# Optimization experiments

Hardware: AMD Instinct MI355X
Metric: run time of the kernel (lower is better)

## Reference

```python
import jax, jax.numpy as jnp
import numpy as np

EMB_DIM = 1024
NUM_HEADS = 16
SCALE_WEIGHTS = 1.0
TINY = jnp.finfo(jnp.float32).tiny


def setup_inputs() -> dict:
    key = jax.random.key(0)
    k1, k2, k3 = jax.random.split(key, 3)
    B, S = 2, 2048
    x = jax.random.normal(k1, (B, S, EMB_DIM), dtype=jnp.float32)
    weights = jax.random.uniform(k2, (B, S), dtype=jnp.float32)
    W_qkv = jax.random.normal(k3, (EMB_DIM, 3 * EMB_DIM), dtype=jnp.float32) / np.sqrt(EMB_DIM)
    b_qkv = jnp.zeros((3 * EMB_DIM,), dtype=jnp.float32)
    return {"x": x, "weights": weights, "W_qkv": W_qkv, "b_qkv": b_qkv}


def reference(x, weights, W_qkv, b_qkv):
    B, S, E = x.shape
    H = NUM_HEADS
    hd = E // H
    # QKV projection: [B,S,3E] -> [B,H,S,3*hd] -> split
    qkv = x @ W_qkv + b_qkv
    qkv = qkv.reshape(B, S, H, 3 * hd).transpose(0, 2, 1, 3)
    q, k, v = jnp.split(qkv, 3, axis=-1)  # each [B,H,S,hd]
    # weights: [B,S] -> [B,1,1,S] (broadcast over heads and query positions)
    w = weights[:, None, None, :]
    # scores with log-weight bias and hard masks
    attn_logits = jnp.einsum("bhqd,bhkd->bhqk", q, k) / jnp.sqrt(jnp.asarray(hd, x.dtype))
    attn_logits = attn_logits + jnp.log(w / SCALE_WEIGHTS + TINY)
    attn_logits = jnp.where(w == 0, -9e15, attn_logits)
    attn_logits = jnp.where(w == 1, 9e15, attn_logits)
    attention = jax.nn.softmax(attn_logits, axis=-1)
    values = jnp.einsum("bhqk,bhkd->bhqd", attention, v)
    return values.transpose(0, 2, 1, 3).reshape(B, S, E)
```

## Files before the change

### kernel.cpp

```cpp
#include <hip/hip_runtime.h>
#include <math.h>

#define B_  2
#define S_  2048
#define E_  1024
#define H_  16
#define HD_ 64
#define N3_ 3072
#define M_  (B_*S_)

typedef _Float16 h8  __attribute__((ext_vector_type(8)));
typedef _Float16 h4  __attribute__((ext_vector_type(4)));
typedef _Float16 h2  __attribute__((ext_vector_type(2)));
typedef __fp16   fp16x2 __attribute__((ext_vector_type(2)));
typedef float    f4  __attribute__((ext_vector_type(4)));
typedef float    fv16 __attribute__((ext_vector_type(16)));

typedef __attribute__((address_space(3))) unsigned int       lds_u32;
typedef const __attribute__((address_space(1))) unsigned int glob_u32;

__device__ __forceinline__ void gld16(const void* g, void* l) {
    __builtin_amdgcn_global_load_lds((glob_u32*)g, (lds_u32*)l, 16, 0, 0);
}
__device__ __forceinline__ float exp2_hw(float x) { return __builtin_amdgcn_exp2f(x); }
__device__ __forceinline__ float fmax3(float a, float b, float c) {
    return fmaxf(fmaxf(a, b), c);
}
__device__ __forceinline__ h2 cvt_pk_f16(float a, float b) {
    fp16x2 r = __builtin_amdgcn_cvt_pkrtz(a, b);
    return __builtin_bit_cast(h2, r);
}

#define QSCALE 0.18033688011112042f
#define RESCALE_THR 8.0f

__global__ __launch_bounds__(256) void prep_kernel(
        const float* __restrict__ x, _Float16* __restrict__ x16,
        const float* __restrict__ w, _Float16* __restrict__ w16,
        const float* __restrict__ W, _Float16* __restrict__ Wt) {
    __shared__ float T[64][65];
    int L = blockIdx.x;
    int tid = threadIdx.x;
    if (L < 2050) {
        const float* src = (L < 2048) ? &x[(size_t)L * 2048] : &w[(size_t)(L - 2048) * 2048];
        _Float16* dst    = (L < 2048) ? &x16[(size_t)L * 2048] : &w16[(size_t)(L - 2048) * 2048];
        int i = tid * 8;
        float4 u = *(const float4*)&src[i];
        float4 v = *(const float4*)&src[i + 4];
        h8 o;
        o[0] = (_Float16)u.x; o[1] = (_Float16)u.y; o[2] = (_Float16)u.z; o[3] = (_Float16)u.w;
        o[4] = (_Float16)v.x; o[5] = (_Float16)v.y; o[6] = (_Float16)v.z; o[7] = (_Float16)v.w;
        *(h8*)&dst[i] = o;
    } else {
        int L2 = L - 2050;
        int k0 = (L2 & 15) * 64, n0 = (L2 >> 4) * 64;
        int r = tid >> 4, c4 = (tid & 15) * 4;
#pragma unroll
        for (int i = 0; i < 4; i++) {
            int row = r + i * 16;
            float4 u = *(const float4*)&W[(size_t)(k0 + row) * N3_ + n0 + c4];
            T[c4 + 0][row] = u.x; T[c4 + 1][row] = u.y;
            T[c4 + 2][row] = u.z; T[c4 + 3][row] = u.w;
        }
        __syncthreads();
#pragma unroll
        for (int i = 0; i < 4; i++) {
            int rn = r + i * 16;
            h4 p;
            p[0] = (_Float16)T[rn][c4 + 0]; p[1] = (_Float16)T[rn][c4 + 1];
            p[2] = (_Float16)T[rn][c4 + 2]; p[3] = (_Float16)T[rn][c4 + 3];
            *(h4*)&Wt[(size_t)(n0 + rn) * E_ + k0 + c4] = p;
        }
    }
}

__global__ __launch_bounds__(256, 2) void qkv_gemm32(
        const _Float16* __restrict__ x16, const _Float16* __restrict__ wt,
        const float* __restrict__ bq, const float* __restrict__ w,
        _Float16* __restrict__ qws, _Float16* __restrict__ kws,
        _Float16* __restrict__ vtws) {
    __shared__ __align__(16) _Float16 Ab[2][128 * 64];
    __shared__ __align__(16) _Float16 Wb[2][192 * 64];

    int tid = threadIdx.x;
    int wid = tid >> 6, lane = tid & 63;
    int l31 = lane & 31, hi = lane >> 5, l7 = l31 & 7;
    int srow = lane >> 3;
    int wm = wid & 1, wn = wid >> 1;

    int L = blockIdx.x;
    int xcd = L & 7;
    int idx = L >> 3;
    int head = (xcd & 1) * 8 + (idx & 7);
    int mb   = (xcd >> 1) * 8 + (idx >> 3);
    int m0 = mb * 128;
    int n0 = head * 192;
    int b = m0 >> 11;
    int bh = b * H_ + head;
    int sblk = m0 & 2047;

    fv16 acc[2][3];
#pragma unroll
    for (int ntl = 0; ntl < 3; ntl++) {
        int n_abs = wn * 96 + ntl * 32;
        int which = n_abs >> 6;
        fv16 ini;
        if (which == 2) {
            float bb = bq[n0 + n_abs + l31];
#pragma unroll
            for (int r = 0; r < 16; r++) ini[r] = bb;
        } else {
#pragma unroll
            for (int g = 0; g < 4; g++) {
                f4 bv = *(const f4*)&bq[n0 + n_abs + 8 * g + 4 * hi];
#pragma unroll
                for (int j = 0; j < 4; j++) ini[4 * g + j] = bv[j];
            }
        }
        acc[0][ntl] = ini; acc[1][ntl] = ini;
    }

    auto stage = [&](int t, int bf) {
        int k0 = t * 64;
#pragma unroll
        for (int j = 0; j < 4; j++) {
            int batch = wid * 4 + j;
            int row = batch * 8 + srow;
            int ch = (lane & 7) ^ srow ^ (batch & 7);
            gld16(&x16[(size_t)(m0 + row) * E_ + k0 + ch * 8], &Ab[bf][batch * 8 * 64]);
        }
#pragma unroll
        for (int j = 0; j < 6; j++) {
            int batch = wid * 6 + j;
            int row = batch * 8 + srow;
            int ch = (lane & 7) ^ srow ^ (batch & 7);
            gld16(&wt[(size_t)(n0 + row) * E_ + k0 + ch * 8], &Wb[bf][batch * 8 * 64]);
        }
    };

    stage(0, 0);

    for (int t = 0; t < 16; t++) {
        int bf = t & 1;
        __syncthreads();
        if (t < 15) stage(t + 1, bf ^ 1);
#pragma unroll
        for (int step = 0; step < 4; step++) {
            h8 af[2], wf[3];
#pragma unroll
            for (int mt = 0; mt < 2; mt++) {
                int R = wm * 64 + mt * 32 + l31;
                int ph = ((2 * step + hi) ^ l7 ^ ((mt * 4 + (l31 >> 3)) & 7)) * 8;
                af[mt] = *(const h8*)&Ab[bf][R * 64 + ph];
            }
#pragma unroll
            for (int ntl = 0; ntl < 3; ntl++) {
                int R = wn * 96 + ntl * 32 + l31;
                int ph = ((2 * step + hi) ^ l7 ^ ((wn * 12 + ntl * 4 + (l31 >> 3)) & 7)) * 8;
                wf[ntl] = *(const h8*)&Wb[bf][R * 64 + ph];
            }
#pragma unroll
            for (int ntl = 0; ntl < 3; ntl++) {
                bool isv = (wn == 1) && (ntl >= 1);
#pragma unroll
                for (int mt = 0; mt < 2; mt++) {
                    if (isv)
                        acc[mt][ntl] = __builtin_amdgcn_mfma_f32_32x32x16_f16(af[mt], wf[ntl], acc[mt][ntl], 0, 0, 0);
                    else
                        acc[mt][ntl] = __builtin_amdgcn_mfma_f32_32x32x16_f16(wf[ntl], af[mt], acc[mt][ntl], 0, 0, 0);
                }
            }
        }
    }

#pragma unroll
    for (int ntl = 0; ntl < 3; ntl++) {
        int n_abs = wn * 96 + ntl * 32;
        int which = n_abs >> 6;
#pragma unroll
        for (int mt = 0; mt < 2; mt++) {
            if (which == 2) {
                int d = (n_abs & 63) + l31;
#pragma unroll
                for (int g = 0; g < 4; g++) {
                    int soff = wm * 64 + mt * 32 + 8 * g + 4 * hi;
                    f4 wf4 = *(const f4*)&w[m0 + soff];
                    h4 p;
#pragma unroll
                    for (int j = 0; j < 4; j++)
                        p[j] = (_Float16)(acc[mt][ntl][4 * g + j] * wf4[j]);
                    *(h4*)&vtws[((size_t)bh * 64 + d) * S_ + sblk + soff] = p;
                }
            } else {
                _Float16* dst = (which == 0) ? qws : kws;
                float scale = (which == 0) ? QSCALE : 1.0f;
                int s = sblk + wm * 64 + mt * 32 + l31;
#pragma unroll
                for (int g = 0; g < 4; g++) {
                    int d0 = (n_abs & 63) + 8 * g + 4 * hi;
                    h4 p;
#pragma unroll
                    for (int j = 0; j < 4; j++)
                        p[j] = (_Float16)(acc[mt][ntl][4 * g + j] * scale);
                    *(h4*)&dst[((size_t)bh * S_ + s) * 64 + d0] = p;
                }
            }
        }
    }
}

__global__ __launch_bounds__(256, 2) void attn_kernel(
        const _Float16* __restrict__ q, const _Float16* __restrict__ k,
        const _Float16* __restrict__ vt, const _Float16* __restrict__ w16,
        float* __restrict__ out) {
    __shared__ __align__(16) _Float16 Kb[2][64 * 64];
    __shared__ __align__(16) _Float16 Vb[2][64 * 64];
    __shared__ __align__(16) _Float16 lws16[2048];

    int tid = threadIdx.x;
    int wid = tid >> 6, lane = tid & 63;
    int l31 = lane & 31, hi = lane >> 5, l7 = l31 & 7;
    int srow = lane >> 3;
    int L = blockIdx.x;
    int bh = (L & 7) + 8 * (L >> 7);
    int qt = (L >> 3) & 15;
    int q0 = qt * 128;
    int b = bh >> 4, h = bh & 15;

    const _Float16* qbase = q + (size_t)bh * S_ * HD_;
    const _Float16* kbase = k + (size_t)bh * S_ * HD_;
    const _Float16* vbase = vt + (size_t)bh * HD_ * S_;
    const _Float16* wbase = w16 + (size_t)b * S_;

    gld16(&wbase[wid * 512 + lane * 8], &lws16[wid * 512]);

    auto stage = [&](int kt, int bf) {
        int k0 = kt * 64;
#pragma unroll
        for (int j = 0; j < 2; j++) {
            int batch = wid * 2 + j;
            int row = batch * 8 + srow;
            int ch = (lane & 7) ^ srow ^ (batch & 7);
            gld16(&kbase[(size_t)(k0 + row) * 64 + ch * 8], &Kb[bf][batch * 8 * 64]);
            gld16(&vbase[(size_t)row * S_ + k0 + ch * 8], &Vb[bf][batch * 8 * 64]);
        }
    };

    stage(0, 0);

    int qrow = q0 + wid * 32 + l31;
    h8 qf[4];
#pragma unroll
    for (int step = 0; step < 4; step++)
        qf[step] = *(const h8*)&qbase[(size_t)qrow * 64 + 16 * step + 8 * hi];

    fv16 o[2], ol;
    o[0] = (fv16)0.0f; o[1] = (fv16)0.0f; ol = (fv16)0.0f;
    float m_r = -INFINITY;

    for (int kt = 0; kt < 32; kt++) {
        int bf = kt & 1;
        __syncthreads();
        if (kt < 31) stage(kt + 1, bf ^ 1);

        fv16 st[2];
        st[0] = (fv16)0.0f; st[1] = (fv16)0.0f;
        __builtin_amdgcn_s_setprio(1);
#pragma unroll
        for (int step = 0; step < 4; step++) {
#pragma unroll
            for (int kt2 = 0; kt2 < 2; kt2++) {
                int R = kt2 * 32 + l31;
                int ph = ((2 * step + hi) ^ l7 ^ ((kt2 * 4 + (l31 >> 3)) & 7)) * 8;
                h8 kf = *(const h8*)&Kb[bf][R * 64 + ph];
                st[kt2] = __builtin_amdgcn_mfma_f32_32x32x16_f16(kf, qf[step], st[kt2], 0, 0, 0);
            }
        }
        __builtin_amdgcn_s_setprio(0);

        float tm[11];
#pragma unroll
        for (int r = 0; r < 10; r++)
            tm[r] = fmax3(st[(3*r)>>4][(3*r)&15], st[(3*r+1)>>4][(3*r+1)&15],
                          st[(3*r+2)>>4][(3*r+2)&15]);
        tm[10] = fmaxf(st[1][14], st[1][15]);
        float u0 = fmax3(tm[0], tm[1], tm[2]);
        float u1 = fmax3(tm[3], tm[4], tm[5]);
        float u2 = fmax3(tm[6], tm[7], tm[8]);
        float u3 = fmaxf(tm[9], tm[10]);
        float pmax = fmaxf(fmax3(u0, u1, u2), u3);

        if (!__all(pmax <= m_r + RESCALE_THR)) {
            float rowmax = fmaxf(pmax, __shfl_xor(pmax, 32));
            float mnew = fmaxf(m_r, rowmax);
            float alpha = exp2_hw(m_r - mnew);
            m_r = mnew;
            o[0] = o[0] * alpha;
            o[1] = o[1] * alpha;
            ol = ol * alpha;
        }

        h4 pf[2][4];
#pragma unroll
        for (int kt2 = 0; kt2 < 2; kt2++)
#pragma unroll
            for (int g = 0; g < 4; g++) {
                float e0 = exp2_hw(st[kt2][4 * g + 0] - m_r);
                float e1 = exp2_hw(st[kt2][4 * g + 1] - m_r);
                float e2 = exp2_hw(st[kt2][4 * g + 2] - m_r);
                float e3 = exp2_hw(st[kt2][4 * g + 3] - m_r);
                h2 p01 = cvt_pk_f16(e0, e1);
                h2 p23 = cvt_pk_f16(e2, e3);
                h4 p;
                p[0] = p01[0]; p[1] = p01[1]; p[2] = p23[0]; p[3] = p23[1];
                pf[kt2][g] = p;
            }

        int k0 = kt * 64;
        __builtin_amdgcn_s_setprio(1);
#pragma unroll
        for (int kt2 = 0; kt2 < 2; kt2++)
#pragma unroll
            for (int g = 0; g < 4; g++) {
                int c = 4 * kt2 + g;
#pragma unroll
                for (int dt = 0; dt < 2; dt++) {
                    int R = dt * 32 + l31;
                    int ph = (c ^ l7 ^ ((dt * 4 + (l31 >> 3)) & 7)) * 8 + hi * 4;
                    h4 vf = *(const h4*)&Vb[bf][R * 64 + ph];
                    o[dt] = __builtin_amdgcn_mfma_f32_32x32x8f16(vf, pf[kt2][g], o[dt], 0, 0, 0);
                }
                h4 wf_ = *(const h4*)&lws16[k0 + c * 8 + 4 * hi];
                ol = __builtin_amdgcn_mfma_f32_32x32x8f16(wf_, pf[kt2][g], ol, 0, 0, 0);
            }
        __builtin_amdgcn_s_setprio(0);
    }

    float linv = 1.0f / ol[0];
    float* obase = &out[((size_t)(b * S_ + qrow)) * E_ + h * 64];
#pragma unroll
    for (int dt = 0; dt < 2; dt++)
#pragma unroll
        for (int g = 0; g < 4; g++) {
            int d0 = dt * 32 + 8 * g + 4 * hi;
            f4 ov;
#pragma unroll
            for (int j = 0; j < 4; j++) ov[j] = o[dt][4 * g + j] * linv;
            *(f4*)&obase[d0] = ov;
        }
}

extern "C" void kernel_launch(void* const* d_in, const int* in_sizes, int n_in,
                              void* d_out, int out_size, void* d_ws, size_t ws_size,
                              hipStream_t stream) {
    const float* x  = (const float*)d_in[0];
    const float* w  = (const float*)d_in[1];
    const float* Wq = (const float*)d_in[2];
    const float* bq = (const float*)d_in[3];
    float* out = (float*)d_out;

    char* p = (char*)d_ws;
    _Float16* x16 = (_Float16*)p;              p += (size_t)M_ * E_ * 2;
    _Float16* wt  = (_Float16*)p;              p += (size_t)E_ * N3_ * 2;
    _Float16* qb  = (_Float16*)p;              p += (size_t)M_ * E_ * 2;
    _Float16* kb  = (_Float16*)p;              p += (size_t)M_ * E_ * 2;
    _Float16* vtb = (_Float16*)p;              p += (size_t)M_ * HD_ * H_ * 2;
    _Float16* w16 = (_Float16*)p;

    prep_kernel<<<dim3(2050 + 768), dim3(256), 0, stream>>>(x, x16, w, w16, Wq, wt);
    qkv_gemm32<<<dim3(512), dim3(256), 0, stream>>>(x16, wt, bq, w, qb, kb, vtb);
    attn_kernel<<<dim3(512), dim3(256), 0, stream>>>(qb, kb, vtb, w16, out);
}
```

Baseline: 177.0 us.

## Split attention KV range across two wave groups per block and merge in LDS

Doubles the attention block to 512 threads and splits the key sequence in two halves, each processed by four waves with their own double-buffered K/V LDS tiles. At the end, partial outputs, maxima and row sums from the second half are written to LDS and merged flash-decoding style by the first half. The aim is more waves in flight per CU and half the serial loop length per block, to hide latency. The cost is double the LDS footprint, an extra merge step, and a tighter register budget from the new launch bounds.

```diff
diff --git a/kernel.cpp b/kernel.cpp
--- a/kernel.cpp
+++ b/kernel.cpp
@@ -209,18 +209,20 @@
     }
 }
 
-__global__ __launch_bounds__(256, 2) void attn_kernel(
+__global__ __launch_bounds__(512, 4) void attn_kernel(
         const _Float16* __restrict__ q, const _Float16* __restrict__ k,
         const _Float16* __restrict__ vt, const _Float16* __restrict__ w16,
         float* __restrict__ out) {
-    __shared__ __align__(16) _Float16 Kb[2][64 * 64];
-    __shared__ __align__(16) _Float16 Vb[2][64 * 64];
+    __shared__ __align__(16) _Float16 Kb[2][2][64 * 64];
+    __shared__ __align__(16) _Float16 Vb[2][2][64 * 64];
     __shared__ __align__(16) _Float16 lws16[2048];
 
     int tid = threadIdx.x;
     int wid = tid >> 6, lane = tid & 63;
     int l31 = lane & 31, hi = lane >> 5, l7 = l31 & 7;
     int srow = lane >> 3;
+    int s = wid >> 2;
+    int w4 = wid & 3;
     int L = blockIdx.x;
     int bh = (L & 7) + 8 * (L >> 7);
     int qt = (L >> 3) & 15;
@@ -232,23 +234,23 @@
     const _Float16* vbase = vt + (size_t)bh * HD_ * S_;
     const _Float16* wbase = w16 + (size_t)b * S_;
 
-    gld16(&wbase[wid * 512 + lane * 8], &lws16[wid * 512]);
-
-    auto stage = [&](int kt, int bf) {
-        int k0 = kt * 64;
+    if (wid < 4) gld16(&wbase[wid * 512 + lane * 8], &lws16[wid * 512]);
+
+    auto stage = [&](int t, int bf) {
+        int k0 = (s * 16 + t) * 64;
 #pragma unroll
         for (int j = 0; j < 2; j++) {
-            int batch = wid * 2 + j;
+            int batch = w4 * 2 + j;
             int row = batch * 8 + srow;
-            int ch = (lane & 7) ^ srow ^ (batch & 7);
-            gld16(&kbase[(size_t)(k0 + row) * 64 + ch * 8], &Kb[bf][batch * 8 * 64]);
-            gld16(&vbase[(size_t)row * S_ + k0 + ch * 8], &Vb[bf][batch * 8 * 64]);
+            int ch = l7 ^ srow ^ (batch & 7);
+            gld16(&kbase[(size_t)(k0 + row) * 64 + ch * 8], &Kb[s][bf][batch * 8 * 64]);
+            gld16(&vbase[(size_t)row * S_ + k0 + ch * 8], &Vb[s][bf][batch * 8 * 64]);
         }
     };
 
     stage(0, 0);
 
-    int qrow = q0 + wid * 32 + l31;
+    int qrow = q0 + w4 * 32 + l31;
     h8 qf[4];
 #pragma unroll
     for (int step = 0; step < 4; step++)
@@ -258,10 +260,10 @@
     o[0] = (fv16)0.0f; o[1] = (fv16)0.0f; ol = (fv16)0.0f;
     float m_r = -INFINITY;
 
-    for (int kt = 0; kt < 32; kt++) {
-        int bf = kt & 1;
+    for (int t = 0; t < 16; t++) {
+        int bf = t & 1;
         __syncthreads();
-        if (kt < 31) stage(kt + 1, bf ^ 1);
+        if (t < 15) stage(t + 1, bf ^ 1);
 
         fv16 st[2];
         st[0] = (fv16)0.0f; st[1] = (fv16)0.0f;
@@ -272,7 +274,7 @@
             for (int kt2 = 0; kt2 < 2; kt2++) {
                 int R = kt2 * 32 + l31;
                 int ph = ((2 * step + hi) ^ l7 ^ ((kt2 * 4 + (l31 >> 3)) & 7)) * 8;
-                h8 kf = *(const h8*)&Kb[bf][R * 64 + ph];
+                h8 kf = *(const h8*)&Kb[s][bf][R * 64 + ph];
                 st[kt2] = __builtin_amdgcn_mfma_f32_32x32x16_f16(kf, qf[step], st[kt2], 0, 0, 0);
             }
         }
@@ -316,7 +318,7 @@
                 pf[kt2][g] = p;
             }
 
-        int k0 = kt * 64;
+        int k0w = (s * 16 + t) * 64;
         __builtin_amdgcn_s_setprio(1);
 #pragma unroll
         for (int kt2 = 0; kt2 < 2; kt2++)
@@ -327,27 +329,53 @@
                 for (int dt = 0; dt < 2; dt++) {
                     int R = dt * 32 + l31;
                     int ph = (c ^ l7 ^ ((dt * 4 + (l31 >> 3)) & 7)) * 8 + hi * 4;
-                    h4 vf = *(const h4*)&Vb[bf][R * 64 + ph];
+                    h4 vf = *(const h4*)&Vb[s][bf][R * 64 + ph];
                     o[dt] = __builtin_amdgcn_mfma_f32_32x32x8f16(vf, pf[kt2][g], o[dt], 0, 0, 0);
                 }
-                h4 wf_ = *(const h4*)&lws16[k0 + c * 8 + 4 * hi];
+                h4 wf_ = *(const h4*)&lws16[k0w + c * 8 + 4 * hi];
                 ol = __builtin_amdgcn_mfma_f32_32x32x8f16(wf_, pf[kt2][g], ol, 0, 0, 0);
             }
         __builtin_amdgcn_s_setprio(0);
     }
 
-    float linv = 1.0f / ol[0];
-    float* obase = &out[((size_t)(b * S_ + qrow)) * E_ + h * 64];
-#pragma unroll
-    for (int dt = 0; dt < 2; dt++)
-#pragma unroll
-        for (int g = 0; g < 4; g++) {
-            int d0 = dt * 32 + 8 * g + 4 * hi;
-            f4 ov;
-#pragma unroll
-            for (int j = 0; j < 4; j++) ov[j] = o[dt][4 * g + j] * linv;
-            *(f4*)&obase[d0] = ov;
-        }
+    float* mO  = (float*)&Kb[0][0][0];
+    float* mML = (float*)&Vb[0][0][0];
+    int qloc = w4 * 32 + l31;
+
+    __syncthreads();
+    if (s == 1) {
+#pragma unroll
+        for (int dt = 0; dt < 2; dt++)
+#pragma unroll
+            for (int r = 0; r < 16; r++) {
+                int d = dt * 32 + (r & 3) + 8 * (r >> 2) + 4 * hi;
+                mO[d * 128 + qloc] = o[dt][r];
+            }
+        if (hi == 0) {
+            mML[qloc * 2]     = m_r;
+            mML[qloc * 2 + 1] = ol[0];
+        }
+    }
+    __syncthreads();
+    if (s == 0) {
+        float m1 = mML[qloc * 2], l1 = mML[qloc * 2 + 1];
+        float mm = fmaxf(m_r, m1);
+        float a0 = exp2_hw(m_r - mm), a1 = exp2_hw(m1 - mm);
+        float linv = 1.0f / (ol[0] * a0 + l1 * a1);
+        a0 *= linv; a1 *= linv;
+        float* obase = &out[((size_t)(b * S_ + q0 + qloc)) * E_ + h * 64];
+#pragma unroll
+        for (int dt = 0; dt < 2; dt++)
+#pragma unroll
+            for (int g = 0; g < 4; g++) {
+                int d0 = dt * 32 + 8 * g + 4 * hi;
+                f4 ov;
+#pragma unroll
+                for (int j = 0; j < 4; j++)
+                    ov[j] = o[dt][4 * g + j] * a0 + mO[(d0 + j) * 128 + qloc] * a1;
+                *(f4*)&obase[d0] = ov;
+            }
+    }
 }
 
 extern "C" void kernel_launch(void* const* d_in, const int* in_sizes, int n_in,
@@ -369,5 +397,5 @@
 
     prep_kernel<<<dim3(2050 + 768), dim3(256), 0, stream>>>(x, x16, w, w16, Wq, wt);
     qkv_gemm32<<<dim3(512), dim3(256), 0, stream>>>(x16, wt, bq, w, qb, kb, vtb);
-    attn_kernel<<<dim3(512), dim3(256), 0, stream>>>(qb, kb, vtb, w16, out);
-}
+    attn_kernel<<<dim3(512), dim3(512), 0, stream>>>(qb, kb, vtb, w16, out);
+}
```

Measured after the change: 188.0 us. +6.2%, slower.

## Load K/V tiles directly from global into registers instead of LDS staging

Applied to the files above, without the earlier changes.

Removes the LDS double-buffered staging of K, V and weights and the per-tile __syncthreads, and has each wave load its MFMA operands directly from global memory into registers. K fragments are register-double-buffered across iterations, and V and weight fragments are loaded inside each tile body. This drops block-wide synchronisation and LDS traffic. The cost is that each wave fetches K/V redundantly instead of sharing one LDS copy, global loads are uncoalesced and partly exposed, and register pressure rises.

```diff
diff --git a/kernel.cpp b/kernel.cpp
--- a/kernel.cpp
+++ b/kernel.cpp
@@ -213,14 +213,9 @@
         const _Float16* __restrict__ q, const _Float16* __restrict__ k,
         const _Float16* __restrict__ vt, const _Float16* __restrict__ w16,
         float* __restrict__ out) {
-    __shared__ __align__(16) _Float16 Kb[2][64 * 64];
-    __shared__ __align__(16) _Float16 Vb[2][64 * 64];
-    __shared__ __align__(16) _Float16 lws16[2048];
-
     int tid = threadIdx.x;
     int wid = tid >> 6, lane = tid & 63;
-    int l31 = lane & 31, hi = lane >> 5, l7 = l31 & 7;
-    int srow = lane >> 3;
+    int l31 = lane & 31, hi = lane >> 5;
     int L = blockIdx.x;
     int bh = (L & 7) + 8 * (L >> 7);
     int qt = (L >> 3) & 15;
@@ -232,22 +227,6 @@
     const _Float16* vbase = vt + (size_t)bh * HD_ * S_;
     const _Float16* wbase = w16 + (size_t)b * S_;
 
-    gld16(&wbase[wid * 512 + lane * 8], &lws16[wid * 512]);
-
-    auto stage = [&](int kt, int bf) {
-        int k0 = kt * 64;
-#pragma unroll
-        for (int j = 0; j < 2; j++) {
-            int batch = wid * 2 + j;
-            int row = batch * 8 + srow;
-            int ch = (lane & 7) ^ srow ^ (batch & 7);
-            gld16(&kbase[(size_t)(k0 + row) * 64 + ch * 8], &Kb[bf][batch * 8 * 64]);
-            gld16(&vbase[(size_t)row * S_ + k0 + ch * 8], &Vb[bf][batch * 8 * 64]);
-        }
-    };
-
-    stage(0, 0);
-
     int qrow = q0 + wid * 32 + l31;
     h8 qf[4];
 #pragma unroll
@@ -258,25 +237,38 @@
     o[0] = (fv16)0.0f; o[1] = (fv16)0.0f; ol = (fv16)0.0f;
     float m_r = -INFINITY;
 
-    for (int kt = 0; kt < 32; kt++) {
-        int bf = kt & 1;
-        __syncthreads();
-        if (kt < 31) stage(kt + 1, bf ^ 1);
-
+    auto loadK = [&](int kt, h8* kr) {
+        int k0 = kt * 64;
+#pragma unroll
+        for (int step = 0; step < 4; step++)
+#pragma unroll
+            for (int kt2 = 0; kt2 < 2; kt2++)
+                kr[step * 2 + kt2] = *(const h8*)
+                    &kbase[(size_t)(k0 + kt2 * 32 + l31) * 64 + 16 * step + 8 * hi];
+    };
+
+    auto body = [&](int kt, const h8* kr) {
         fv16 st[2];
         st[0] = (fv16)0.0f; st[1] = (fv16)0.0f;
         __builtin_amdgcn_s_setprio(1);
 #pragma unroll
-        for (int step = 0; step < 4; step++) {
-#pragma unroll
-            for (int kt2 = 0; kt2 < 2; kt2++) {
-                int R = kt2 * 32 + l31;
-                int ph = ((2 * step + hi) ^ l7 ^ ((kt2 * 4 + (l31 >> 3)) & 7)) * 8;
-                h8 kf = *(const h8*)&Kb[bf][R * 64 + ph];
-                st[kt2] = __builtin_amdgcn_mfma_f32_32x32x16_f16(kf, qf[step], st[kt2], 0, 0, 0);
-            }
-        }
+        for (int step = 0; step < 4; step++)
+#pragma unroll
+            for (int kt2 = 0; kt2 < 2; kt2++)
+                st[kt2] = __builtin_amdgcn_mfma_f32_32x32x16_f16(
+                    kr[step * 2 + kt2], qf[step], st[kt2], 0, 0, 0);
         __builtin_amdgcn_s_setprio(0);
+
+        int k0 = kt * 64;
+        h4 vf[2][8], wfv[8];
+#pragma unroll
+        for (int c = 0; c < 8; c++) {
+#pragma unroll
+            for (int dt = 0; dt < 2; dt++)
+                vf[dt][c] = *(const h4*)
+                    &vbase[(size_t)(dt * 32 + l31) * S_ + k0 + c * 8 + hi * 4];
+            wfv[c] = *(const h4*)&wbase[k0 + c * 8 + hi * 4];
+        }
 
         float tm[11];
 #pragma unroll
@@ -316,7 +308,6 @@
                 pf[kt2][g] = p;
             }
 
-        int k0 = kt * 64;
         __builtin_amdgcn_s_setprio(1);
 #pragma unroll
         for (int kt2 = 0; kt2 < 2; kt2++)
@@ -324,16 +315,20 @@
             for (int g = 0; g < 4; g++) {
                 int c = 4 * kt2 + g;
 #pragma unroll
-                for (int dt = 0; dt < 2; dt++) {
-                    int R = dt * 32 + l31;
-                    int ph = (c ^ l7 ^ ((dt * 4 + (l31 >> 3)) & 7)) * 8 + hi * 4;
-                    h4 vf = *(const h4*)&Vb[bf][R * 64 + ph];
-                    o[dt] = __builtin_amdgcn_mfma_f32_32x32x8f16(vf, pf[kt2][g], o[dt], 0, 0, 0);
-                }
-                h4 wf_ = *(const h4*)&lws16[k0 + c * 8 + 4 * hi];
-                ol = __builtin_amdgcn_mfma_f32_32x32x8f16(wf_, pf[kt2][g], ol, 0, 0, 0);
+                for (int dt = 0; dt < 2; dt++)
+                    o[dt] = __builtin_amdgcn_mfma_f32_32x32x8f16(vf[dt][c], pf[kt2][g], o[dt], 0, 0, 0);
+                ol = __builtin_amdgcn_mfma_f32_32x32x8f16(wfv[c], pf[kt2][g], ol, 0, 0, 0);
             }
         __builtin_amdgcn_s_setprio(0);
+    };
+
+    h8 kA[8], kB[8];
+    loadK(0, kA);
+    for (int it = 0; it < 16; it++) {
+        loadK(2 * it + 1, kB);
+        body(2 * it, kA);
+        if (it < 15) loadK(2 * it + 2, kA);
+        body(2 * it + 1, kB);
     }
 
     float linv = 1.0f / ol[0];
```

New measurement: 298.0 us. +68.4%, slower.
